# Performance work log

Hardware: AMD Instinct MI355X
Metric: run time of the kernel (lower is better)

## Reference

```python
import jax, jax.numpy as jnp
import numpy as np

B, N, FIN, H, D = 2, 512, 128, 4, 64
NEG_SLOPE = 0.2


def setup_inputs() -> dict:
    key = jax.random.key(0)
    ks = jax.random.split(key, 5)
    x = jax.random.normal(ks[0], (B, N, FIN), dtype=jnp.float32)
    # xavier-ish scaled params
    W_proj = jax.random.normal(ks[1], (H, FIN, D), dtype=jnp.float32) * (1.0 / np.sqrt(FIN + D))
    b_proj = jnp.zeros((H, D), dtype=jnp.float32)
    W_cat_weight = jax.random.normal(ks[2], (H, D, 2 * D), dtype=jnp.float32) * (1.0 / np.sqrt(3 * D))
    W_cat_bias = jnp.zeros((H, D), dtype=jnp.float32)
    a = jax.random.normal(ks[3], (H, D), dtype=jnp.float32) * (1.0 / np.sqrt(D))
    bias_param = jnp.zeros((H * D,), dtype=jnp.float32)
    return {"x": x, "W_proj": W_proj, "b_proj": b_proj,
            "W_cat_weight": W_cat_weight, "W_cat_bias": W_cat_bias,
            "a": a, "bias_param": bias_param}


def reference(x, W_proj, b_proj, W_cat_weight, W_cat_bias, a, bias_param):
    # h[b,h,n,d] = W^h x_n + b^h
    h = jnp.einsum('bni,hid->bhnd', x, W_proj) + b_proj[None, :, None, :]
    d = h.shape[-1]
    # W_cat [h_i || h_j] == W1 h_i + W2 h_j  (avoids O(N^2*2D) concat tensor)
    W1 = W_cat_weight[:, :, :d]   # (H, D, D) acts on source node i
    W2 = W_cat_weight[:, :, d:]   # (H, D, D) acts on target node j
    zi = jnp.einsum('bhnd,hed->bhne', h, W1)  # (B,H,N,D)
    zj = jnp.einsum('bhnd,hed->bhne', h, W2)  # (B,H,N,D)
    # z[b,h,i,j,e] = zi[b,h,i,e] + zj[b,h,j,e] + bias, then LeakyReLU
    z = zi[:, :, :, None, :] + zj[:, :, None, :, :] + W_cat_bias[None, :, None, None, :]
    z = jnp.where(z >= 0, z, NEG_SLOPE * z)
    # e[b,h,i,j] = a_h . z
    e = jnp.einsum('bhije,he->bhij', z, a)
    attn = jax.nn.softmax(e, axis=-1)          # softmax over neighbors j
    out = jnp.einsum('bhij,bhjd->bhid', attn, h)  # (B,H,N,D)
    b_, h_, n_, d_ = out.shape
    out = out.transpose(0, 2, 1, 3).reshape(b_, n_, h_ * d_)  # concat heads
    out = out + bias_param
    return out
```

## Files before the change

### kernel.cpp

```cpp
#include <hip/hip_runtime.h>
#include <hip/hip_bf16.h>

#define NN 512
#define FIN 128
#define HH 4
#define DD 64


__device__ __forceinline__ float rdlane(float v, int idx) {
    return __int_as_float(__builtin_amdgcn_readlane(__float_as_int(v), idx));
}

__global__ __launch_bounds__(256) void proj_kernel(
    const float* __restrict__ x, const float* __restrict__ Wp,
    const float* __restrict__ bp, const float* __restrict__ Wc,
    const float* __restrict__ Wcb, const float* __restrict__ a,
    float* __restrict__ h_ws, float* __restrict__ zi_ws, float* __restrict__ zj_ws,
    float* __restrict__ adi_ws, float* __restrict__ adj_ws)
{
    int blk = blockIdx.x;
    int bh = blk >> 6;
    int n0 = (blk & 63) << 3;
    int b = bh >> 2, hh = bh & 3;

    __shared__ float xs[8 * FIN];
    __shared__ float hs[8][DD];
    __shared__ float Wcs[DD][2 * DD + 1];

    int t = threadIdx.x;

    ((float4*)xs)[t] = ((const float4*)(x + ((size_t)b * NN + n0) * FIN))[t];
    {
        const float4* wg = (const float4*)(Wc + (size_t)hh * DD * 2 * DD);
        #pragma unroll
        for (int k = 0; k < 8; ++k) {
            int idx = t + 256 * k;
            int r = idx >> 5, c4 = (idx & 31) * 4;
            float4 v = wg[idx];
            Wcs[r][c4] = v.x; Wcs[r][c4 + 1] = v.y;
            Wcs[r][c4 + 2] = v.z; Wcs[r][c4 + 3] = v.w;
        }
    }
    __syncthreads();

    int e = t & 63, w = t >> 6;
    const float* Wph = Wp + (size_t)hh * FIN * DD;
    float bpv = bp[hh * DD + e];
    float acc0 = bpv, acc1 = bpv;
    #pragma unroll 8
    for (int i = 0; i < FIN; ++i) {
        float wv = Wph[i * DD + e];
        acc0 = fmaf(xs[w * FIN + i], wv, acc0);
        acc1 = fmaf(xs[(w + 4) * FIN + i], wv, acc1);
    }
    hs[w][e] = acc0; hs[w + 4][e] = acc1;
    float* hg = h_ws + ((size_t)bh * NN + n0) * DD;
    hg[w * DD + e] = acc0; hg[(w + 4) * DD + e] = acc1;
    __syncthreads();

    float zb = Wcb[hh * DD + e];
    float zi0 = zb, zi1 = zb, zj0 = 0.f, zj1 = 0.f;
    #pragma unroll 8
    for (int d2 = 0; d2 < DD; ++d2) {
        float w1 = Wcs[e][d2];
        float w2 = Wcs[e][DD + d2];
        float h0 = hs[w][d2], h1 = hs[w + 4][d2];
        zi0 = fmaf(h0, w1, zi0); zi1 = fmaf(h1, w1, zi1);
        zj0 = fmaf(h0, w2, zj0); zj1 = fmaf(h1, w2, zj1);
    }

    float* zib = zi_ws + ((size_t)bh * NN + n0) * DD;
    float* zjb = zj_ws + ((size_t)bh * NN + n0) * DD;
    zib[w * DD + e] = zi0; zib[(w + 4) * DD + e] = zi1;
    zjb[w * DD + e] = zj0; zjb[(w + 4) * DD + e] = zj1;

    float av = a[hh * DD + e];
    float p0 = av * zi0, p1 = av * zi1, q0 = av * zj0, q1 = av * zj1;
    #pragma unroll
    for (int off = 32; off; off >>= 1) {
        p0 += __shfl_xor(p0, off); p1 += __shfl_xor(p1, off);
        q0 += __shfl_xor(q0, off); q1 += __shfl_xor(q1, off);
    }
    if (e == 0) {
        adi_ws[bh * NN + n0 + w]     = 0.6f * p0;
        adi_ws[bh * NN + n0 + w + 4] = 0.6f * p1;
        adj_ws[bh * NN + n0 + w]     = 0.6f * q0;
        adj_ws[bh * NN + n0 + w + 4] = 0.6f * q1;
    }
}

__global__ __launch_bounds__(256) void attn7(
    const float* __restrict__ h_ws, const float* __restrict__ zi_ws,
    const float* __restrict__ zj_ws, const float* __restrict__ adi_ws,
    const float* __restrict__ adj_ws, const float* __restrict__ a,
    float* __restrict__ pacc, float* __restrict__ pm, float* __restrict__ ps)
{
    int blk = blockIdx.x;
    int js = blk & 15, is_ = (blk >> 4) & 7, bh = blk >> 7;
    int i0 = is_ << 6, j0 = js << 5, hh = bh & 3;
    int t = threadIdx.x, lane = t & 63, w = t >> 6;

    __shared__ float eP[32 * 65];

    float4 zi4[16];
    {
        const float4* zr = (const float4*)(zi_ws + ((size_t)bh * NN + i0 + lane) * DD);
        #pragma unroll
        for (int k = 0; k < 16; ++k) zi4[k] = zr[k];
    }
    float vu   = 0.4f * a[hh * DD + lane];
    float vadj = adj_ws[bh * NN + j0 + (lane & 31)];
    float vadi = adi_ws[bh * NN + i0 + lane];

    #pragma unroll
    for (int jj = 0; jj < 8; ++jj) {
        int j = 8 * w + jj;
        float vzj = zj_ws[((size_t)bh * NN + j0 + j) * DD + lane];
        float sadj = rdlane(vadj, j);
        float a0 = 0.f, a1 = 0.f, a2 = 0.f, a3 = 0.f;
        #pragma unroll
        for (int k = 0; k < 16; ++k) {
            float4 z = zi4[k];
            float s0 = rdlane(vzj, 4 * k + 0), u0 = rdlane(vu, 4 * k + 0);
            float s1 = rdlane(vzj, 4 * k + 1), u1 = rdlane(vu, 4 * k + 1);
            float s2 = rdlane(vzj, 4 * k + 2), u2 = rdlane(vu, 4 * k + 2);
            float s3 = rdlane(vzj, 4 * k + 3), u3 = rdlane(vu, 4 * k + 3);
            a0 = fmaf(u0, __builtin_fabsf(z.x + s0), a0);
            a1 = fmaf(u1, __builtin_fabsf(z.y + s1), a1);
            a2 = fmaf(u2, __builtin_fabsf(z.z + s2), a2);
            a3 = fmaf(u3, __builtin_fabsf(z.w + s3), a3);
        }
        eP[j * 65 + lane] = vadi + sadj + ((a0 + a1) + (a2 + a3));
    }
    __syncthreads();

    {
        int il = lane & 15, jq = lane >> 4;
        int iL = 16 * w + il;
        float e8[8];
        float m = -1e30f;
        #pragma unroll
        for (int jj = 0; jj < 8; ++jj) {
            e8[jj] = eP[(jq * 8 + jj) * 65 + iL];
            m = fmaxf(m, e8[jj]);
        }
        m = fmaxf(m, __shfl_xor(m, 16));
        m = fmaxf(m, __shfl_xor(m, 32));
        float s = 0.f;
        #pragma unroll
        for (int jj = 0; jj < 8; ++jj) {
            float p = __expf(e8[jj] - m);
            s += p;
            eP[(jq * 8 + jj) * 65 + iL] = p;
        }
        s += __shfl_xor(s, 16);
        s += __shfl_xor(s, 32);
        if (jq == 0) {
            pm[js * 4096 + bh * NN + i0 + iL] = m;
            ps[js * 4096 + bh * NN + i0 + iL] = s;
        }
    }
    __syncthreads();

    float acc[16];
    #pragma unroll
    for (int ii = 0; ii < 16; ++ii) acc[ii] = 0.f;
    #pragma unroll 8
    for (int j = 0; j < 32; ++j) {
        float vh = h_ws[((size_t)bh * NN + j0 + j) * DD + lane];
        float vp = eP[j * 65 + lane];
        #pragma unroll
        for (int ii = 0; ii < 16; ++ii) {
            float sp = rdlane(vp, 16 * w + ii);
            acc[ii] = fmaf(sp, vh, acc[ii]);
        }
    }

    float* pb = pacc + ((size_t)(js * 8 + bh) * NN + i0 + 16 * w) * DD + lane;
    #pragma unroll
    for (int ii = 0; ii < 16; ++ii)
        pb[(size_t)ii * DD] = acc[ii];
}

__global__ __launch_bounds__(256) void combine_kernel(
    const float* __restrict__ pacc, const float* __restrict__ pm,
    const float* __restrict__ ps, const float* __restrict__ bias_param,
    float* __restrict__ out)
{
    int tid = blockIdx.x * 256 + threadIdx.x;
    int d = tid & 63;
    int row = tid >> 6;
    int bh = row >> 9, n = row & 511;
    int b = bh >> 2, hh = bh & 3;
    float mv[16];
    float m = -1e30f;
    #pragma unroll
    for (int p = 0; p < 16; ++p) { mv[p] = pm[p * 4096 + row]; m = fmaxf(m, mv[p]); }
    float denom = 0.f, acc = 0.f;
    #pragma unroll
    for (int p = 0; p < 16; ++p) {
        float wgt = __expf(mv[p] - m);
        denom = fmaf(ps[p * 4096 + row], wgt, denom);
        acc = fmaf(pacc[(size_t)p * 262144 + (size_t)row * 64 + d], wgt, acc);
    }
    out[((size_t)b * NN + n) * (HH * DD) + hh * DD + d] =
        acc / denom + bias_param[hh * DD + d];
}

extern "C" void kernel_launch(void* const* d_in, const int* in_sizes, int n_in,
                              void* d_out, int out_size, void* d_ws, size_t ws_size,
                              hipStream_t stream) {
    const float* x    = (const float*)d_in[0];
    const float* Wp   = (const float*)d_in[1];
    const float* bp   = (const float*)d_in[2];
    const float* Wc   = (const float*)d_in[3];
    const float* Wcb  = (const float*)d_in[4];
    const float* a    = (const float*)d_in[5];
    const float* bpar = (const float*)d_in[6];
    float* out = (float*)d_out;

    float* ws     = (float*)d_ws;
    float* h_ws   = ws;
    float* zi_ws  = ws + 262144;
    float* zj_ws  = ws + 524288;
    float* adi_ws = ws + 786432;
    float* adj_ws = ws + 790528;
    float* pacc   = ws + 794624;
    float* pm     = ws + 4988928;
    float* ps     = ws + 5054464;

    proj_kernel<<<dim3(512), dim3(256), 0, stream>>>(
        x, Wp, bp, Wc, Wcb, a, h_ws, zi_ws, zj_ws, adi_ws, adj_ws);
    attn7<<<dim3(1024), dim3(256), 0, stream>>>(
        h_ws, zi_ws, zj_ws, adi_ws, adj_ws, a, pacc, pm, ps);
    combine_kernel<<<dim3(1024), dim3(256), 0, stream>>>(
        pacc, pm, ps, bpar, out);
}
```

Measured before the change: 54.06 us.

## Enlarge attention i-tile to 128 rows and stage zj/h tiles in LDS

The attention kernel now processes 128 query rows per block instead of 64, halving the grid. Each thread holds two zi rows in registers so every zj element fetched from shared memory is reused twice. zj and h tiles are staged in LDS and the per-lane readlane broadcasts of zj and a are replaced by hoisted scalars and LDS float4 reads. Softmax probabilities are written to a global scratch buffer and read back as float4 for the P·H product. This removes readlane overhead and improves reuse, at the cost of heavy register pressure (two 64-float zi arrays plus 64 hoisted scalars), half as many blocks, and extra global traffic through the scratch buffer.

```diff
diff --git a/kernel.cpp b/kernel.cpp
--- a/kernel.cpp
+++ b/kernel.cpp
@@ -89,97 +89,129 @@
     }
 }
 
-__global__ __launch_bounds__(256) void attn7(
+__global__ __launch_bounds__(256) void attn8(
     const float* __restrict__ h_ws, const float* __restrict__ zi_ws,
     const float* __restrict__ zj_ws, const float* __restrict__ adi_ws,
     const float* __restrict__ adj_ws, const float* __restrict__ a,
-    float* __restrict__ pacc, float* __restrict__ pm, float* __restrict__ ps)
+    float* __restrict__ pacc, float* __restrict__ pm, float* __restrict__ ps,
+    float* __restrict__ p_ws)
 {
     int blk = blockIdx.x;
-    int js = blk & 15, is_ = (blk >> 4) & 7, bh = blk >> 7;
-    int i0 = is_ << 6, j0 = js << 5, hh = bh & 3;
-    int t = threadIdx.x, lane = t & 63, w = t >> 6;
-
-    __shared__ float eP[32 * 65];
-
-    float4 zi4[16];
-    {
-        const float4* zr = (const float4*)(zi_ws + ((size_t)bh * NN + i0 + lane) * DD);
-        #pragma unroll
-        for (int k = 0; k < 16; ++k) zi4[k] = zr[k];
-    }
-    float vu   = 0.4f * a[hh * DD + lane];
+    int js = blk & 15, is_ = (blk >> 4) & 3, bh = blk >> 6;
+    int i0 = is_ << 7, j0 = js << 5, hh = bh & 3;
+    int t = threadIdx.x, lane = t & 63;
+    int wid = __builtin_amdgcn_readfirstlane(t >> 6);
+
+    __shared__ float smZJ[32 * 64];
+    __shared__ float smH[32 * 64];
+    __shared__ float eL[32 * 129];
+
+    float4 ziA[16], ziB[16];
+    {
+        const float4* zr0 = (const float4*)(zi_ws + ((size_t)bh * NN + i0 + lane) * DD);
+        const float4* zr1 = (const float4*)(zi_ws + ((size_t)bh * NN + i0 + 64 + lane) * DD);
+        #pragma unroll
+        for (int k = 0; k < 16; ++k) { ziA[k] = zr0[k]; ziB[k] = zr1[k]; }
+    }
+
+    {
+        const float4* sj = (const float4*)(zj_ws + ((size_t)bh * NN + j0) * DD);
+        const float4* sh = (const float4*)(h_ws + ((size_t)bh * NN + j0) * DD);
+        ((float4*)smZJ)[t] = sj[t];
+        ((float4*)smZJ)[t + 256] = sj[t + 256];
+        ((float4*)smH)[t] = sh[t];
+        ((float4*)smH)[t + 256] = sh[t + 256];
+    }
+
+    float vu = 0.4f * a[hh * DD + lane];
+    float us[64];
+    #pragma unroll
+    for (int k = 0; k < 64; ++k) us[k] = rdlane(vu, k);
+
     float vadj = adj_ws[bh * NN + j0 + (lane & 31)];
-    float vadi = adi_ws[bh * NN + i0 + lane];
+    float adjS[8];
+    #pragma unroll
+    for (int jj = 0; jj < 8; ++jj) adjS[jj] = rdlane(vadj, 8 * wid + jj);
+
+    float adi0 = adi_ws[bh * NN + i0 + lane];
+    float adi1 = adi_ws[bh * NN + i0 + 64 + lane];
+
+    __syncthreads();
 
     #pragma unroll
     for (int jj = 0; jj < 8; ++jj) {
-        int j = 8 * w + jj;
-        float vzj = zj_ws[((size_t)bh * NN + j0 + j) * DD + lane];
-        float sadj = rdlane(vadj, j);
-        float a0 = 0.f, a1 = 0.f, a2 = 0.f, a3 = 0.f;
+        int j = 8 * wid + jj;
+        const float4* zjr = (const float4*)(smZJ + j * 64);
+        float a0 = 0.f, a1 = 0.f, b0 = 0.f, b1 = 0.f;
         #pragma unroll
         for (int k = 0; k < 16; ++k) {
-            float4 z = zi4[k];
-            float s0 = rdlane(vzj, 4 * k + 0), u0 = rdlane(vu, 4 * k + 0);
-            float s1 = rdlane(vzj, 4 * k + 1), u1 = rdlane(vu, 4 * k + 1);
-            float s2 = rdlane(vzj, 4 * k + 2), u2 = rdlane(vu, 4 * k + 2);
-            float s3 = rdlane(vzj, 4 * k + 3), u3 = rdlane(vu, 4 * k + 3);
-            a0 = fmaf(u0, __builtin_fabsf(z.x + s0), a0);
-            a1 = fmaf(u1, __builtin_fabsf(z.y + s1), a1);
-            a2 = fmaf(u2, __builtin_fabsf(z.z + s2), a2);
-            a3 = fmaf(u3, __builtin_fabsf(z.w + s3), a3);
-        }
-        eP[j * 65 + lane] = vadi + sadj + ((a0 + a1) + (a2 + a3));
-    }
-    __syncthreads();
-
-    {
-        int il = lane & 15, jq = lane >> 4;
-        int iL = 16 * w + il;
-        float e8[8];
+            float4 z = zjr[k];
+            float u0 = us[4 * k], u1 = us[4 * k + 1];
+            float u2 = us[4 * k + 2], u3 = us[4 * k + 3];
+            a0 = fmaf(u0, __builtin_fabsf(ziA[k].x + z.x), a0);
+            a1 = fmaf(u1, __builtin_fabsf(ziA[k].y + z.y), a1);
+            a0 = fmaf(u2, __builtin_fabsf(ziA[k].z + z.z), a0);
+            a1 = fmaf(u3, __builtin_fabsf(ziA[k].w + z.w), a1);
+            b0 = fmaf(u0, __builtin_fabsf(ziB[k].x + z.x), b0);
+            b1 = fmaf(u1, __builtin_fabsf(ziB[k].y + z.y), b1);
+            b0 = fmaf(u2, __builtin_fabsf(ziB[k].z + z.z), b0);
+            b1 = fmaf(u3, __builtin_fabsf(ziB[k].w + z.w), b1);
+        }
+        eL[j * 129 + lane]      = adi0 + adjS[jj] + (a0 + a1);
+        eL[j * 129 + 64 + lane] = adi1 + adjS[jj] + (b0 + b1);
+    }
+    __syncthreads();
+
+    {
+        int r = t >> 1, jh = t & 1;
+        float e16[16];
         float m = -1e30f;
         #pragma unroll
-        for (int jj = 0; jj < 8; ++jj) {
-            e8[jj] = eP[(jq * 8 + jj) * 65 + iL];
-            m = fmaxf(m, e8[jj]);
-        }
-        m = fmaxf(m, __shfl_xor(m, 16));
-        m = fmaxf(m, __shfl_xor(m, 32));
+        for (int jj = 0; jj < 16; ++jj) {
+            e16[jj] = eL[(16 * jh + jj) * 129 + r];
+            m = fmaxf(m, e16[jj]);
+        }
+        m = fmaxf(m, __shfl_xor(m, 1));
         float s = 0.f;
-        #pragma unroll
-        for (int jj = 0; jj < 8; ++jj) {
-            float p = __expf(e8[jj] - m);
+        float* pb = p_ws + (size_t)blk * 4096 + 16 * jh * 128 + r;
+        #pragma unroll
+        for (int jj = 0; jj < 16; ++jj) {
+            float p = __expf(e16[jj] - m);
             s += p;
-            eP[(jq * 8 + jj) * 65 + iL] = p;
-        }
-        s += __shfl_xor(s, 16);
-        s += __shfl_xor(s, 32);
-        if (jq == 0) {
-            pm[js * 4096 + bh * NN + i0 + iL] = m;
-            ps[js * 4096 + bh * NN + i0 + iL] = s;
-        }
-    }
-    __syncthreads();
-
-    float acc[16];
-    #pragma unroll
-    for (int ii = 0; ii < 16; ++ii) acc[ii] = 0.f;
-    #pragma unroll 8
-    for (int j = 0; j < 32; ++j) {
-        float vh = h_ws[((size_t)bh * NN + j0 + j) * DD + lane];
-        float vp = eP[j * 65 + lane];
-        #pragma unroll
-        for (int ii = 0; ii < 16; ++ii) {
-            float sp = rdlane(vp, 16 * w + ii);
-            acc[ii] = fmaf(sp, vh, acc[ii]);
-        }
-    }
-
-    float* pb = pacc + ((size_t)(js * 8 + bh) * NN + i0 + 16 * w) * DD + lane;
-    #pragma unroll
-    for (int ii = 0; ii < 16; ++ii)
-        pb[(size_t)ii * DD] = acc[ii];
+            pb[jj * 128] = p;
+        }
+        s += __shfl_xor(s, 1);
+        if (jh == 0) {
+            pm[js * 4096 + bh * NN + i0 + r] = m;
+            ps[js * 4096 + bh * NN + i0 + r] = s;
+        }
+    }
+    __syncthreads();
+
+    {
+        int ib = 32 * wid;
+        float acc[32];
+        #pragma unroll
+        for (int q = 0; q < 32; ++q) acc[q] = 0.f;
+        const float* pbase = p_ws + (size_t)blk * 4096 + ib;
+        #pragma unroll 4
+        for (int j = 0; j < 32; ++j) {
+            float hv = smH[j * 64 + lane];
+            const float4* pw = (const float4*)(pbase + j * 128);
+            #pragma unroll
+            for (int q4 = 0; q4 < 8; ++q4) {
+                float4 pv = pw[q4];
+                acc[4 * q4 + 0] = fmaf(pv.x, hv, acc[4 * q4 + 0]);
+                acc[4 * q4 + 1] = fmaf(pv.y, hv, acc[4 * q4 + 1]);
+                acc[4 * q4 + 2] = fmaf(pv.z, hv, acc[4 * q4 + 2]);
+                acc[4 * q4 + 3] = fmaf(pv.w, hv, acc[4 * q4 + 3]);
+            }
+        }
+        float* ob = pacc + ((size_t)(js * 8 + bh) * NN + i0 + ib) * DD + lane;
+        #pragma unroll
+        for (int q = 0; q < 32; ++q)
+            ob[(size_t)q * DD] = acc[q];
+    }
 }
 
 __global__ __launch_bounds__(256) void combine_kernel(
@@ -228,11 +260,12 @@
     float* pacc   = ws + 794624;
     float* pm     = ws + 4988928;
     float* ps     = ws + 5054464;
+    float* p_ws   = ws + 5120000;
 
     proj_kernel<<<dim3(512), dim3(256), 0, stream>>>(
         x, Wp, bp, Wc, Wcb, a, h_ws, zi_ws, zj_ws, adi_ws, adj_ws);
-    attn7<<<dim3(1024), dim3(256), 0, stream>>>(
-        h_ws, zi_ws, zj_ws, adi_ws, adj_ws, a, pacc, pm, ps);
+    attn8<<<dim3(512), dim3(256), 0, stream>>>(
+        h_ws, zi_ws, zj_ws, adi_ws, adj_ws, a, pacc, pm, ps, p_ws);
     combine_kernel<<<dim3(1024), dim3(256), 0, stream>>>(
         pacc, pm, ps, bpar, out);
 }
```

New measurement: 53.16 us. Within noise of the previous version (-1.7%).
